# Optimization experiments

Measured on AMD Instinct MI355X. Metric: run time of the kernel, lower is better.

## Reference

```python
import jax, jax.numpy as jnp
import numpy as np

N_NODES = 10000
N_EDGES = 640000
D = 128


def setup_inputs() -> dict:
    key = jax.random.key(0)
    ks = jax.random.split(key, 8)
    x = jax.random.normal(ks[0], (N_NODES, D), dtype=jnp.float32)
    edge_weight = jax.random.uniform(ks[1], (N_EDGES,), dtype=jnp.float32)
    W0 = jax.random.normal(ks[2], (D, D), dtype=jnp.float32) * (1.0 / np.sqrt(D))
    b0 = jnp.zeros((D,), dtype=jnp.float32)
    W1 = jax.random.normal(ks[3], (D, D), dtype=jnp.float32) * (1.0 / np.sqrt(D))
    b1 = jnp.zeros((D,), dtype=jnp.float32)
    src = jax.random.randint(ks[4], (N_EDGES,), 0, N_NODES)
    dst = jax.random.randint(ks[5], (N_EDGES,), 0, N_NODES)
    return {"x": x, "edge_weight": edge_weight, "W0": W0, "b0": b0,
            "W1": W1, "b1": b1, "src": src, "dst": dst}


def _graph_conv(h, src, dst, edge_weight, W, b):
    # DGL GraphConv with norm='both', bias, activation=relu.
    n = h.shape[0]
    ones = jnp.ones((src.shape[0],), dtype=h.dtype)
    out_deg = jax.ops.segment_sum(ones, src, num_segments=n)
    in_deg = jax.ops.segment_sum(ones, dst, num_segments=n)
    norm_src = jax.lax.rsqrt(jnp.maximum(out_deg, 1.0))  # [N]
    norm_dst = jax.lax.rsqrt(jnp.maximum(in_deg, 1.0))   # [N]
    h = h * norm_src[:, None]
    # gather -> weight edges -> scatter-add (sparse neighbor aggregation)
    msg = h[src] * edge_weight[:, None]                  # [E, D]
    agg = jax.ops.segment_sum(msg, dst, num_segments=n)  # [N, D]
    rst = agg @ W                                        # in_feats == out_feats: aggregate first
    rst = rst * norm_dst[:, None] + b
    return jax.nn.relu(rst)  # activation inside GraphConv


def reference(x, edge_weight, W0, b0, W1, b1, src, dst):
    # NET.forward (full-graph path): per layer GraphConv -> activation -> dropout.
    # Dropout is identity in eval mode; outer relu after GraphConv's internal relu is idempotent
    # but applied for faithfulness.
    h = jax.nn.relu(_graph_conv(x, src, dst, edge_weight, W0, b0))
    h = jax.nn.relu(_graph_conv(h, src, dst, edge_weight, W1, b1))
    return h  # predict is None (n_classes=None)
```

## Files before the change

kernel.cpp:

```cpp
#include <hip/hip_runtime.h>
#include <hip/hip_fp16.h>

#define D 128
#define NB 256
#define Q 8
#define BQ (NB / Q)
#define NBINS_MAX 10016
#define GM 32

__global__ __launch_bounds__(256) void cast_kernel(const float* __restrict__ x, __half* __restrict__ xh, int total4) {
    int i = blockIdx.x * 256 + threadIdx.x;
    if (i >= total4) return;
    float4 v = *(const float4*)(x + (size_t)i * 4);
    __half2 a = __floats2half2_rn(v.x, v.y);
    __half2 b = __floats2half2_rn(v.z, v.w);
    *(__half2*)(xh + (size_t)i * 4) = a;
    *(__half2*)(xh + (size_t)i * 4 + 2) = b;
}

__global__ __launch_bounds__(256) void hist_kernel(const int* __restrict__ src, const int* __restrict__ dst,
                                                   int* __restrict__ pd, unsigned short* __restrict__ ps,
                                                   int E, int n) {
    __shared__ int hd[NBINS_MAX];
    __shared__ int hs[NBINS_MAX];
    int b = blockIdx.x, t = threadIdx.x;
    int chunk = (E + NB - 1) / NB;
    int e0 = b * chunk, e1 = min(e0 + chunk, E);
    for (int i = t; i < n; i += 256) { hd[i] = 0; hs[i] = 0; }
    __syncthreads();
    for (int e = e0 + t; e < e1; e += 256) {
        atomicAdd(&hd[dst[e]], 1);
        atomicAdd(&hs[src[e]], 1);
    }
    __syncthreads();
    for (int i = t; i < n; i += 256) {
        pd[(size_t)b * n + i] = hd[i];
        ps[(size_t)b * n + i] = (unsigned short)hs[i];
    }
}

__global__ __launch_bounds__(256) void colscan_kernel(int* __restrict__ pd, const unsigned short* __restrict__ ps,
                                                      int* __restrict__ qtot_d, int* __restrict__ qtot_s, int n) {
    int bin = blockIdx.x * 256 + threadIdx.x;
    int q = blockIdx.y;
    if (bin >= n) return;
    int b0 = q * BQ;
    int run = 0, ssum = 0;
#pragma unroll 8
    for (int j = 0; j < BQ; ++j) {
        size_t idx = (size_t)(b0 + j) * n + bin;
        int v = pd[idx];
        pd[idx] = run;
        run += v;
        ssum += (int)ps[idx];
    }
    qtot_d[(size_t)q * n + bin] = run;
    qtot_s[(size_t)q * n + bin] = ssum;
}

__global__ __launch_bounds__(256) void finalize_kernel(int* __restrict__ qtot_d ,
                                                       const int* __restrict__ qtot_s,
                                                       int* __restrict__ in_deg,
                                                       float* __restrict__ norm_src, float* __restrict__ norm_dst,
                                                       int n) {
    int bin = blockIdx.x * 256 + threadIdx.x;
    if (bin >= n) return;
    int run = 0;
#pragma unroll
    for (int q = 0; q < Q; ++q) {
        size_t i = (size_t)q * n + bin;
        int v = qtot_d[i];
        qtot_d[i] = run;
        run += v;
    }
    in_deg[bin] = run;
    norm_dst[bin] = rsqrtf(fmaxf((float)run, 1.0f));
    int tot = 0;
#pragma unroll
    for (int q = 0; q < Q; ++q) tot += qtot_s[(size_t)q * n + bin];
    norm_src[bin] = rsqrtf(fmaxf((float)tot, 1.0f));
}

__global__ __launch_bounds__(1024) void scan_kernel(const int* __restrict__ in_deg, int* __restrict__ row_start, int n) {
    __shared__ int buf[NBINS_MAX];
    __shared__ int part[1024];
    int t = threadIdx.x;
    for (int i = t; i < n; i += 1024) buf[i] = in_deg[i];
    __syncthreads();
    int ipt = (n + 1023) / 1024;
    int lo = min(t * ipt, n), hi = min(lo + ipt, n);
    int s = 0;
    for (int i = lo; i < hi; ++i) s += buf[i];
    part[t] = s;
    __syncthreads();
    for (int off = 1; off < 1024; off <<= 1) {
        int v = 0;
        if (t >= off) v = part[t - off];
        __syncthreads();
        if (t >= off) part[t] += v;
        __syncthreads();
    }
    int run = part[t] - s;
    for (int i = lo; i < hi; ++i) {
        int v = buf[i];
        buf[i] = run;
        run += v;
    }
    __syncthreads();
    for (int i = t; i < n; i += 1024) row_start[i] = buf[i];
    if (t == 0) row_start[n] = part[1023];
}

__global__ __launch_bounds__(256) void fill_kernel(const int* __restrict__ src, const int* __restrict__ dst,
                                                   const float* __restrict__ ew, const float* __restrict__ ns,
                                                   const int* __restrict__ row_start, const int* __restrict__ qbase,
                                                   const int* __restrict__ pd,
                                                   int2* __restrict__ sorted, int E, int n) {
    __shared__ int cursor[NBINS_MAX];
    int b = blockIdx.x, t = threadIdx.x;
    int q = b / BQ;
    int chunk = (E + NB - 1) / NB;
    int e0 = b * chunk, e1 = min(e0 + chunk, E);
    for (int i = t; i < n; i += 256)
        cursor[i] = row_start[i] + qbase[(size_t)q * n + i] + pd[(size_t)b * n + i];
    __syncthreads();
    for (int e = e0 + t; e < e1; e += 256) {
        int d = dst[e];
        int slot = atomicAdd(&cursor[d], 1);
        int s = src[e];
        int2 rec;
        rec.x = s;
        rec.y = __float_as_int(ew[e] * ns[s]);
        sorted[slot] = rec;
    }
}

__global__ __launch_bounds__(256) void agg_kernel(const __half* __restrict__ h, const int* __restrict__ row_start,
                                                  const int2* __restrict__ sorted, float* __restrict__ out,
                                                  int n, int qn) {
    int slot  = blockIdx.x & 7;
    int g     = blockIdx.x >> 3;
    int chunk = slot >> 2;
    int quad  = slot & 3;
    int wave  = threadIdx.x >> 6;
    int lane  = threadIdx.x & 63;
    int node  = quad * qn + g * 4 + wave;
    int hiN   = min((quad + 1) * qn, n);
    if (node >= hiN) return;
    const __half* hc = h + chunk * 64 + lane;
    int beg = __builtin_amdgcn_readfirstlane(row_start[node]);
    int end = __builtin_amdgcn_readfirstlane(row_start[node + 1]);
    float acc = 0.f;
    int s = beg;
    if (s < end && (s & 1)) {
        int2 rr = sorted[s];
        acc = fmaf(__int_as_float(rr.y), __half2float(hc[(size_t)rr.x << 7]), acc);
        ++s;
    }
    int4 p0, p1, p2, p3, p4, p5, p6, p7;
    if (s + 16 <= end) {
        p0 = *(const int4*)(sorted + s);
        p1 = *(const int4*)(sorted + s + 2);
        p2 = *(const int4*)(sorted + s + 4);
        p3 = *(const int4*)(sorted + s + 6);
        p4 = *(const int4*)(sorted + s + 8);
        p5 = *(const int4*)(sorted + s + 10);
        p6 = *(const int4*)(sorted + s + 12);
        p7 = *(const int4*)(sorted + s + 14);
    }
    for (; s + 32 <= end; s += 16) {
        int4 q0 = *(const int4*)(sorted + s + 16);
        int4 q1 = *(const int4*)(sorted + s + 18);
        int4 q2 = *(const int4*)(sorted + s + 20);
        int4 q3 = *(const int4*)(sorted + s + 22);
        int4 q4 = *(const int4*)(sorted + s + 24);
        int4 q5 = *(const int4*)(sorted + s + 26);
        int4 q6 = *(const int4*)(sorted + s + 28);
        int4 q7 = *(const int4*)(sorted + s + 30);
        __half x0  = hc[(size_t)p0.x << 7];
        __half x1  = hc[(size_t)p0.z << 7];
        __half x2  = hc[(size_t)p1.x << 7];
        __half x3  = hc[(size_t)p1.z << 7];
        __half x4  = hc[(size_t)p2.x << 7];
        __half x5  = hc[(size_t)p2.z << 7];
        __half x6  = hc[(size_t)p3.x << 7];
        __half x7  = hc[(size_t)p3.z << 7];
        __half x8  = hc[(size_t)p4.x << 7];
        __half x9  = hc[(size_t)p4.z << 7];
        __half x10 = hc[(size_t)p5.x << 7];
        __half x11 = hc[(size_t)p5.z << 7];
        __half x12 = hc[(size_t)p6.x << 7];
        __half x13 = hc[(size_t)p6.z << 7];
        __half x14 = hc[(size_t)p7.x << 7];
        __half x15 = hc[(size_t)p7.z << 7];
        acc = fmaf(__int_as_float(p0.y), __half2float(x0),  acc);
        acc = fmaf(__int_as_float(p0.w), __half2float(x1),  acc);
        acc = fmaf(__int_as_float(p1.y), __half2float(x2),  acc);
        acc = fmaf(__int_as_float(p1.w), __half2float(x3),  acc);
        acc = fmaf(__int_as_float(p2.y), __half2float(x4),  acc);
        acc = fmaf(__int_as_float(p2.w), __half2float(x5),  acc);
        acc = fmaf(__int_as_float(p3.y), __half2float(x6),  acc);
        acc = fmaf(__int_as_float(p3.w), __half2float(x7),  acc);
        acc = fmaf(__int_as_float(p4.y), __half2float(x8),  acc);
        acc = fmaf(__int_as_float(p4.w), __half2float(x9),  acc);
        acc = fmaf(__int_as_float(p5.y), __half2float(x10), acc);
        acc = fmaf(__int_as_float(p5.w), __half2float(x11), acc);
        acc = fmaf(__int_as_float(p6.y), __half2float(x12), acc);
        acc = fmaf(__int_as_float(p6.w), __half2float(x13), acc);
        acc = fmaf(__int_as_float(p7.y), __half2float(x14), acc);
        acc = fmaf(__int_as_float(p7.w), __half2float(x15), acc);
        p0 = q0; p1 = q1; p2 = q2; p3 = q3;
        p4 = q4; p5 = q5; p6 = q6; p7 = q7;
    }
    if (s + 16 <= end) {
        acc = fmaf(__int_as_float(p0.y), __half2float(hc[(size_t)p0.x << 7]), acc);
        acc = fmaf(__int_as_float(p0.w), __half2float(hc[(size_t)p0.z << 7]), acc);
        acc = fmaf(__int_as_float(p1.y), __half2float(hc[(size_t)p1.x << 7]), acc);
        acc = fmaf(__int_as_float(p1.w), __half2float(hc[(size_t)p1.z << 7]), acc);
        acc = fmaf(__int_as_float(p2.y), __half2float(hc[(size_t)p2.x << 7]), acc);
        acc = fmaf(__int_as_float(p2.w), __half2float(hc[(size_t)p2.z << 7]), acc);
        acc = fmaf(__int_as_float(p3.y), __half2float(hc[(size_t)p3.x << 7]), acc);
        acc = fmaf(__int_as_float(p3.w), __half2float(hc[(size_t)p3.z << 7]), acc);
        acc = fmaf(__int_as_float(p4.y), __half2float(hc[(size_t)p4.x << 7]), acc);
        acc = fmaf(__int_as_float(p4.w), __half2float(hc[(size_t)p4.z << 7]), acc);
        acc = fmaf(__int_as_float(p5.y), __half2float(hc[(size_t)p5.x << 7]), acc);
        acc = fmaf(__int_as_float(p5.w), __half2float(hc[(size_t)p5.z << 7]), acc);
        acc = fmaf(__int_as_float(p6.y), __half2float(hc[(size_t)p6.x << 7]), acc);
        acc = fmaf(__int_as_float(p6.w), __half2float(hc[(size_t)p6.z << 7]), acc);
        acc = fmaf(__int_as_float(p7.y), __half2float(hc[(size_t)p7.x << 7]), acc);
        acc = fmaf(__int_as_float(p7.w), __half2float(hc[(size_t)p7.z << 7]), acc);
        s += 16;
    }
    if (s + 8 <= end) {
        int4 a0 = *(const int4*)(sorted + s);
        int4 a1 = *(const int4*)(sorted + s + 2);
        int4 a2 = *(const int4*)(sorted + s + 4);
        int4 a3 = *(const int4*)(sorted + s + 6);
        acc = fmaf(__int_as_float(a0.y), __half2float(hc[(size_t)a0.x << 7]), acc);
        acc = fmaf(__int_as_float(a0.w), __half2float(hc[(size_t)a0.z << 7]), acc);
        acc = fmaf(__int_as_float(a1.y), __half2float(hc[(size_t)a1.x << 7]), acc);
        acc = fmaf(__int_as_float(a1.w), __half2float(hc[(size_t)a1.z << 7]), acc);
        acc = fmaf(__int_as_float(a2.y), __half2float(hc[(size_t)a2.x << 7]), acc);
        acc = fmaf(__int_as_float(a2.w), __half2float(hc[(size_t)a2.z << 7]), acc);
        acc = fmaf(__int_as_float(a3.y), __half2float(hc[(size_t)a3.x << 7]), acc);
        acc = fmaf(__int_as_float(a3.w), __half2float(hc[(size_t)a3.z << 7]), acc);
        s += 8;
    }
    for (; s + 2 <= end; s += 2) {
        int4 p = *(const int4*)(sorted + s);
        acc = fmaf(__int_as_float(p.y), __half2float(hc[(size_t)p.x << 7]), acc);
        acc = fmaf(__int_as_float(p.w), __half2float(hc[(size_t)p.z << 7]), acc);
    }
    if (s < end) {
        int2 rr = sorted[s];
        acc = fmaf(__int_as_float(rr.y), __half2float(hc[(size_t)rr.x << 7]), acc);
    }
    out[((size_t)node << 7) + chunk * 64 + lane] = acc;
}

template <int HALF_OUT>
__global__ __launch_bounds__(256) void gemm_kernel(const float* __restrict__ A, const float* __restrict__ W,
                                                   const float* __restrict__ bias, const float* __restrict__ norm_dst,
                                                   float* __restrict__ out, __half* __restrict__ out_h, int n) {
    __shared__ __align__(16) float sAT[D][GM + 2];
    int tid = threadIdx.x;
    int row0 = blockIdx.x * GM;
    for (int i = tid; i < GM * 32; i += 256) {
        int r = i >> 5;
        int kq = i & 31;
        int rr = row0 + r;
        float4 v = make_float4(0.f, 0.f, 0.f, 0.f);
        if (rr < n) v = *(const float4*)(A + (size_t)rr * D + kq * 4);
        sAT[kq * 4 + 0][r] = v.x;
        sAT[kq * 4 + 1][r] = v.y;
        sAT[kq * 4 + 2][r] = v.z;
        sAT[kq * 4 + 3][r] = v.w;
    }
    __syncthreads();
    int tx = tid & 15;
    int ty = tid >> 4;
    int c0 = tx * 8;
    int r0 = ty * 2;
    float acc0[8], acc1[8];
#pragma unroll
    for (int j = 0; j < 8; ++j) { acc0[j] = 0.f; acc1[j] = 0.f; }
    const float* Wk = W + c0;
#pragma unroll 4
    for (int k = 0; k < D; ++k) {
        float2 a = *(const float2*)&sAT[k][r0];
        float4 w0 = *(const float4*)(Wk);
        float4 w1 = *(const float4*)(Wk + 4);
        Wk += D;
        acc0[0] = fmaf(a.x, w0.x, acc0[0]);
        acc0[1] = fmaf(a.x, w0.y, acc0[1]);
        acc0[2] = fmaf(a.x, w0.z, acc0[2]);
        acc0[3] = fmaf(a.x, w0.w, acc0[3]);
        acc0[4] = fmaf(a.x, w1.x, acc0[4]);
        acc0[5] = fmaf(a.x, w1.y, acc0[5]);
        acc0[6] = fmaf(a.x, w1.z, acc0[6]);
        acc0[7] = fmaf(a.x, w1.w, acc0[7]);
        acc1[0] = fmaf(a.y, w0.x, acc1[0]);
        acc1[1] = fmaf(a.y, w0.y, acc1[1]);
        acc1[2] = fmaf(a.y, w0.z, acc1[2]);
        acc1[3] = fmaf(a.y, w0.w, acc1[3]);
        acc1[4] = fmaf(a.y, w1.x, acc1[4]);
        acc1[5] = fmaf(a.y, w1.y, acc1[5]);
        acc1[6] = fmaf(a.y, w1.z, acc1[6]);
        acc1[7] = fmaf(a.y, w1.w, acc1[7]);
    }
#pragma unroll 2
    for (int rr = 0; rr < 2; ++rr) {
        int r = row0 + r0 + rr;
        if (r >= n) continue;
        float* acc = rr ? acc1 : acc0;
        float nd = norm_dst[r];
        float o[8];
#pragma unroll
        for (int j = 0; j < 8; ++j) o[j] = fmaxf(fmaf(acc[j], nd, bias[c0 + j]), 0.f);
        if (HALF_OUT) {
            __half2 h0 = __floats2half2_rn(o[0], o[1]);
            __half2 h1 = __floats2half2_rn(o[2], o[3]);
            __half2 h2 = __floats2half2_rn(o[4], o[5]);
            __half2 h3 = __floats2half2_rn(o[6], o[7]);
            __half* p = out_h + (size_t)r * D + c0;
            *(__half2*)(p + 0) = h0;
            *(__half2*)(p + 2) = h1;
            *(__half2*)(p + 4) = h2;
            *(__half2*)(p + 6) = h3;
        } else {
            float4 o0 = make_float4(o[0], o[1], o[2], o[3]);
            float4 o1 = make_float4(o[4], o[5], o[6], o[7]);
            *(float4*)(out + (size_t)r * D + c0) = o0;
            *(float4*)(out + (size_t)r * D + c0 + 4) = o1;
        }
    }
}

extern "C" void kernel_launch(void* const* d_in, const int* in_sizes, int n_in,
                              void* d_out, int out_size, void* d_ws, size_t ws_size,
                              hipStream_t stream) {
    const float* x  = (const float*)d_in[0];
    const float* ew = (const float*)d_in[1];
    const float* W0 = (const float*)d_in[2];
    const float* b0 = (const float*)d_in[3];
    const float* W1 = (const float*)d_in[4];
    const float* b1 = (const float*)d_in[5];
    const int* src  = (const int*)d_in[6];
    const int* dst  = (const int*)d_in[7];
    float* out = (float*)d_out;

    int n = in_sizes[0] / D;
    int E = in_sizes[6];
    if (n <= 0 || E <= 0) return;

    char* ws = (char*)d_ws;
    size_t off = 0;
    auto alloc = [&](size_t bytes) -> void* {
        void* p = ws + off;
        off = (off + bytes + 255) & ~(size_t)255;
        return p;
    };
    int* row_start  = (int*)alloc(((size_t)n + 1) * 4);
    int* in_deg     = (int*)alloc((size_t)n * 4);
    float* norm_src = (float*)alloc((size_t)n * 4);
    float* norm_dst = (float*)alloc((size_t)n * 4);
    int* qtot_d     = (int*)alloc((size_t)Q * n * 4);
    int* qtot_s     = (int*)alloc((size_t)Q * n * 4);
    int2* sorted    = (int2*)alloc((size_t)E * 8);
    int* pd         = (int*)alloc((size_t)NB * n * 4);
    unsigned short* ps = (unsigned short*)alloc((size_t)NB * n * 2);
    float* B1       = (float*)alloc((size_t)n * D * 4);
    __half* xh      = (__half*)alloc((size_t)n * D * 2);
    __half* B2h     = (__half*)alloc((size_t)n * D * 2);

    int nb = (n + 255) / 256;
    int qn = (n + 3) / 4;
    int ab = 8 * ((qn + 3) / 4);
    int gb = (n + GM - 1) / GM;
    int cb = ((n * D / 4) + 255) / 256;

    cast_kernel<<<cb, 256, 0, stream>>>(x, xh, n * D / 4);
    hist_kernel<<<NB, 256, 0, stream>>>(src, dst, pd, ps, E, n);
    colscan_kernel<<<dim3(nb, Q), 256, 0, stream>>>(pd, ps, qtot_d, qtot_s, n);
    finalize_kernel<<<nb, 256, 0, stream>>>(qtot_d, qtot_s, in_deg, norm_src, norm_dst, n);
    scan_kernel<<<1, 1024, 0, stream>>>(in_deg, row_start, n);
    fill_kernel<<<NB, 256, 0, stream>>>(src, dst, ew, norm_src, row_start, qtot_d, pd, sorted, E, n);

    agg_kernel<<<ab, 256, 0, stream>>>(xh, row_start, sorted, B1, n, qn);
    gemm_kernel<1><<<gb, 256, 0, stream>>>(B1, W0, b0, norm_dst, nullptr, B2h, n);
    agg_kernel<<<ab, 256, 0, stream>>>(B2h, row_start, sorted, B1, n, qn);
    gemm_kernel<0><<<gb, 256, 0, stream>>>(B1, W1, b1, norm_dst, out, nullptr, n);
}
```

Measured before the change: 188.5 us.

## Fuse neighbor aggregation and dense GEMM into one per-layer kernel

Aggregation results for a 32-node tile are now written straight into shared memory and consumed by the GEMM epilogue in the same block, replacing the separate agg and gemm kernels. This removes the fp32 intermediate buffer round-trip through global memory and two kernel launches. Blocks grow to 512 threads, with each wave handling 8 row-chunk tasks serially. The grid shrinks to about 313 blocks, and the old node-quadrant interleaving across blocks is gone, which may reduce latency hiding and load balance for the gather phase.

```diff
diff --git a/kernel.cpp b/kernel.cpp
--- a/kernel.cpp
+++ b/kernel.cpp
@@ -135,21 +135,8 @@
     }
 }
 
-__global__ __launch_bounds__(256) void agg_kernel(const __half* __restrict__ h, const int* __restrict__ row_start,
-                                                  const int2* __restrict__ sorted, float* __restrict__ out,
-                                                  int n, int qn) {
-    int slot  = blockIdx.x & 7;
-    int g     = blockIdx.x >> 3;
-    int chunk = slot >> 2;
-    int quad  = slot & 3;
-    int wave  = threadIdx.x >> 6;
-    int lane  = threadIdx.x & 63;
-    int node  = quad * qn + g * 4 + wave;
-    int hiN   = min((quad + 1) * qn, n);
-    if (node >= hiN) return;
-    const __half* hc = h + chunk * 64 + lane;
-    int beg = __builtin_amdgcn_readfirstlane(row_start[node]);
-    int end = __builtin_amdgcn_readfirstlane(row_start[node + 1]);
+__device__ __forceinline__ float agg_row(const __half* __restrict__ hc, const int2* __restrict__ sorted,
+                                         int beg, int end) {
     float acc = 0.f;
     int s = beg;
     if (s < end && (s & 1)) {
@@ -255,64 +242,59 @@
         int2 rr = sorted[s];
         acc = fmaf(__int_as_float(rr.y), __half2float(hc[(size_t)rr.x << 7]), acc);
     }
-    out[((size_t)node << 7) + chunk * 64 + lane] = acc;
+    return acc;
 }
 
 template <int HALF_OUT>
-__global__ __launch_bounds__(256) void gemm_kernel(const float* __restrict__ A, const float* __restrict__ W,
-                                                   const float* __restrict__ bias, const float* __restrict__ norm_dst,
-                                                   float* __restrict__ out, __half* __restrict__ out_h, int n) {
+__global__ __launch_bounds__(512) void fused_kernel(const __half* __restrict__ h, const int* __restrict__ row_start,
+                                                    const int2* __restrict__ sorted,
+                                                    const float* __restrict__ W, const float* __restrict__ bias,
+                                                    const float* __restrict__ norm_dst,
+                                                    float* __restrict__ out, __half* __restrict__ out_h, int n) {
     __shared__ __align__(16) float sAT[D][GM + 2];
-    int tid = threadIdx.x;
+    int tid  = threadIdx.x;
+    int wave = tid >> 6;
+    int lane = tid & 63;
     int row0 = blockIdx.x * GM;
-    for (int i = tid; i < GM * 32; i += 256) {
-        int r = i >> 5;
-        int kq = i & 31;
-        int rr = row0 + r;
-        float4 v = make_float4(0.f, 0.f, 0.f, 0.f);
-        if (rr < n) v = *(const float4*)(A + (size_t)rr * D + kq * 4);
-        sAT[kq * 4 + 0][r] = v.x;
-        sAT[kq * 4 + 1][r] = v.y;
-        sAT[kq * 4 + 2][r] = v.z;
-        sAT[kq * 4 + 3][r] = v.w;
+#pragma unroll 1
+    for (int t = 0; t < 8; ++t) {
+        int task  = wave * 8 + t;
+        int r     = task & 31;
+        int chunk = task >> 5;
+        int node  = row0 + r;
+        if (node < n) {
+            const __half* hc = h + chunk * 64 + lane;
+            int beg = __builtin_amdgcn_readfirstlane(row_start[node]);
+            int end = __builtin_amdgcn_readfirstlane(row_start[node + 1]);
+            float acc = agg_row(hc, sorted, beg, end);
+            sAT[chunk * 64 + lane][r] = acc;
+        }
     }
     __syncthreads();
     int tx = tid & 15;
     int ty = tid >> 4;
     int c0 = tx * 8;
-    int r0 = ty * 2;
-    float acc0[8], acc1[8];
+    float acc[8];
 #pragma unroll
-    for (int j = 0; j < 8; ++j) { acc0[j] = 0.f; acc1[j] = 0.f; }
+    for (int j = 0; j < 8; ++j) acc[j] = 0.f;
     const float* Wk = W + c0;
 #pragma unroll 4
     for (int k = 0; k < D; ++k) {
-        float2 a = *(const float2*)&sAT[k][r0];
+        float a = sAT[k][ty];
         float4 w0 = *(const float4*)(Wk);
         float4 w1 = *(const float4*)(Wk + 4);
         Wk += D;
-        acc0[0] = fmaf(a.x, w0.x, acc0[0]);
-        acc0[1] = fmaf(a.x, w0.y, acc0[1]);
-        acc0[2] = fmaf(a.x, w0.z, acc0[2]);
-        acc0[3] = fmaf(a.x, w0.w, acc0[3]);
-        acc0[4] = fmaf(a.x, w1.x, acc0[4]);
-        acc0[5] = fmaf(a.x, w1.y, acc0[5]);
-        acc0[6] = fmaf(a.x, w1.z, acc0[6]);
-        acc0[7] = fmaf(a.x, w1.w, acc0[7]);
-        acc1[0] = fmaf(a.y, w0.x, acc1[0]);
-        acc1[1] = fmaf(a.y, w0.y, acc1[1]);
-        acc1[2] = fmaf(a.y, w0.z, acc1[2]);
-        acc1[3] = fmaf(a.y, w0.w, acc1[3]);
-        acc1[4] = fmaf(a.y, w1.x, acc1[4]);
-        acc1[5] = fmaf(a.y, w1.y, acc1[5]);
-        acc1[6] = fmaf(a.y, w1.z, acc1[6]);
-        acc1[7] = fmaf(a.y, w1.w, acc1[7]);
-    }
-#pragma unroll 2
-    for (int rr = 0; rr < 2; ++rr) {
-        int r = row0 + r0 + rr;
-        if (r >= n) continue;
-        float* acc = rr ? acc1 : acc0;
+        acc[0] = fmaf(a, w0.x, acc[0]);
+        acc[1] = fmaf(a, w0.y, acc[1]);
+        acc[2] = fmaf(a, w0.z, acc[2]);
+        acc[3] = fmaf(a, w0.w, acc[3]);
+        acc[4] = fmaf(a, w1.x, acc[4]);
+        acc[5] = fmaf(a, w1.y, acc[5]);
+        acc[6] = fmaf(a, w1.z, acc[6]);
+        acc[7] = fmaf(a, w1.w, acc[7]);
+    }
+    int r = row0 + ty;
+    if (r < n) {
         float nd = norm_dst[r];
         float o[8];
 #pragma unroll
@@ -328,10 +310,8 @@
             *(__half2*)(p + 4) = h2;
             *(__half2*)(p + 6) = h3;
         } else {
-            float4 o0 = make_float4(o[0], o[1], o[2], o[3]);
-            float4 o1 = make_float4(o[4], o[5], o[6], o[7]);
-            *(float4*)(out + (size_t)r * D + c0) = o0;
-            *(float4*)(out + (size_t)r * D + c0 + 4) = o1;
+            *(float4*)(out + (size_t)r * D + c0)     = make_float4(o[0], o[1], o[2], o[3]);
+            *(float4*)(out + (size_t)r * D + c0 + 4) = make_float4(o[4], o[5], o[6], o[7]);
         }
     }
 }
@@ -369,13 +349,10 @@
     int2* sorted    = (int2*)alloc((size_t)E * 8);
     int* pd         = (int*)alloc((size_t)NB * n * 4);
     unsigned short* ps = (unsigned short*)alloc((size_t)NB * n * 2);
-    float* B1       = (float*)alloc((size_t)n * D * 4);
     __half* xh      = (__half*)alloc((size_t)n * D * 2);
     __half* B2h     = (__half*)alloc((size_t)n * D * 2);
 
     int nb = (n + 255) / 256;
-    int qn = (n + 3) / 4;
-    int ab = 8 * ((qn + 3) / 4);
     int gb = (n + GM - 1) / GM;
     int cb = ((n * D / 4) + 255) / 256;
 
@@ -386,8 +363,6 @@
     scan_kernel<<<1, 1024, 0, stream>>>(in_deg, row_start, n);
     fill_kernel<<<NB, 256, 0, stream>>>(src, dst, ew, norm_src, row_start, qtot_d, pd, sorted, E, n);
 
-    agg_kernel<<<ab, 256, 0, stream>>>(xh, row_start, sorted, B1, n, qn);
-    gemm_kernel<1><<<gb, 256, 0, stream>>>(B1, W0, b0, norm_dst, nullptr, B2h, n);
-    agg_kernel<<<ab, 256, 0, stream>>>(B2h, row_start, sorted, B1, n, qn);
-    gemm_kernel<0><<<gb, 256, 0, stream>>>(B1, W1, b1, norm_dst, out, nullptr, n);
-}
+    fused_kernel<1><<<gb, 512, 0, stream>>>(xh, row_start, sorted, W0, b0, norm_dst, nullptr, B2h, n);
+    fused_kernel<0><<<gb, 512, 0, stream>>>(B2h, row_start, sorted, W1, b1, norm_dst, out, nullptr, n);
+}
```

Result: slower. 237.9 us (+26.2%).

## Fuse degree finalize and row scan into one decoupled-lookback kernel, vectorize histogram passes

Applied to the files above, without the earlier changes.

Merges the finalize and single-block scan kernels into one multi-block scan. Blocks chain their prefix through a global counter with spin-waiting, and the kernel also writes per-quarter row bases so fill_kernel no longer adds row_start. The histogram, column-scan and fill cursor setup now use int4 vectorized accesses, so colscan gets four bins per thread. This cuts one launch and the serial 1024-thread scan, but the spin-wait assumes blocks are scheduled in order and needs a memset of the counter.

```diff
diff --git a/kernel.cpp b/kernel.cpp
--- a/kernel.cpp
+++ b/kernel.cpp
@@ -21,19 +21,33 @@
 __global__ __launch_bounds__(256) void hist_kernel(const int* __restrict__ src, const int* __restrict__ dst,
                                                    int* __restrict__ pd, unsigned short* __restrict__ ps,
                                                    int E, int n) {
-    __shared__ int hd[NBINS_MAX];
-    __shared__ int hs[NBINS_MAX];
+    __shared__ __align__(16) int hd[NBINS_MAX];
+    __shared__ __align__(16) int hs[NBINS_MAX];
     int b = blockIdx.x, t = threadIdx.x;
     int chunk = (E + NB - 1) / NB;
     int e0 = b * chunk, e1 = min(e0 + chunk, E);
-    for (int i = t; i < n; i += 256) { hd[i] = 0; hs[i] = 0; }
+    int nq = (n + 3) >> 2;
+    for (int i = t; i < nq; i += 256) {
+        *(int4*)(&hd[i * 4]) = make_int4(0, 0, 0, 0);
+        *(int4*)(&hs[i * 4]) = make_int4(0, 0, 0, 0);
+    }
     __syncthreads();
     for (int e = e0 + t; e < e1; e += 256) {
         atomicAdd(&hd[dst[e]], 1);
         atomicAdd(&hs[src[e]], 1);
     }
     __syncthreads();
-    for (int i = t; i < n; i += 256) {
+    int nf = n >> 2;
+    for (int i = t; i < nf; i += 256) {
+        int4 h = *(const int4*)(&hd[i * 4]);
+        *(int4*)(pd + (size_t)b * n + i * 4) = h;
+        int4 s = *(const int4*)(&hs[i * 4]);
+        uint2 u;
+        u.x = (unsigned)(s.x & 0xFFFF) | ((unsigned)(s.y & 0xFFFF) << 16);
+        u.y = (unsigned)(s.z & 0xFFFF) | ((unsigned)(s.w & 0xFFFF) << 16);
+        *(uint2*)(ps + (size_t)b * n + i * 4) = u;
+    }
+    for (int i = nf * 4 + t; i < n; i += 256) {
         pd[(size_t)b * n + i] = hd[i];
         ps[(size_t)b * n + i] = (unsigned short)hs[i];
     }
@@ -41,88 +55,144 @@
 
 __global__ __launch_bounds__(256) void colscan_kernel(int* __restrict__ pd, const unsigned short* __restrict__ ps,
                                                       int* __restrict__ qtot_d, int* __restrict__ qtot_s, int n) {
-    int bin = blockIdx.x * 256 + threadIdx.x;
+    int bin4 = (blockIdx.x * 256 + threadIdx.x) * 4;
     int q = blockIdx.y;
-    if (bin >= n) return;
+    if (bin4 >= n) return;
     int b0 = q * BQ;
-    int run = 0, ssum = 0;
+    if (bin4 + 3 < n) {
+        int4 run = make_int4(0, 0, 0, 0);
+        int4 ssum = make_int4(0, 0, 0, 0);
 #pragma unroll 8
-    for (int j = 0; j < BQ; ++j) {
-        size_t idx = (size_t)(b0 + j) * n + bin;
-        int v = pd[idx];
-        pd[idx] = run;
-        run += v;
-        ssum += (int)ps[idx];
-    }
-    qtot_d[(size_t)q * n + bin] = run;
-    qtot_s[(size_t)q * n + bin] = ssum;
-}
-
-__global__ __launch_bounds__(256) void finalize_kernel(int* __restrict__ qtot_d ,
-                                                       const int* __restrict__ qtot_s,
-                                                       int* __restrict__ in_deg,
-                                                       float* __restrict__ norm_src, float* __restrict__ norm_dst,
-                                                       int n) {
-    int bin = blockIdx.x * 256 + threadIdx.x;
-    if (bin >= n) return;
-    int run = 0;
-#pragma unroll
-    for (int q = 0; q < Q; ++q) {
-        size_t i = (size_t)q * n + bin;
-        int v = qtot_d[i];
-        qtot_d[i] = run;
-        run += v;
-    }
-    in_deg[bin] = run;
-    norm_dst[bin] = rsqrtf(fmaxf((float)run, 1.0f));
-    int tot = 0;
-#pragma unroll
-    for (int q = 0; q < Q; ++q) tot += qtot_s[(size_t)q * n + bin];
-    norm_src[bin] = rsqrtf(fmaxf((float)tot, 1.0f));
-}
-
-__global__ __launch_bounds__(1024) void scan_kernel(const int* __restrict__ in_deg, int* __restrict__ row_start, int n) {
-    __shared__ int buf[NBINS_MAX];
-    __shared__ int part[1024];
-    int t = threadIdx.x;
-    for (int i = t; i < n; i += 1024) buf[i] = in_deg[i];
-    __syncthreads();
-    int ipt = (n + 1023) / 1024;
-    int lo = min(t * ipt, n), hi = min(lo + ipt, n);
-    int s = 0;
-    for (int i = lo; i < hi; ++i) s += buf[i];
-    part[t] = s;
-    __syncthreads();
-    for (int off = 1; off < 1024; off <<= 1) {
-        int v = 0;
-        if (t >= off) v = part[t - off];
+        for (int j = 0; j < BQ; ++j) {
+            size_t idx = (size_t)(b0 + j) * n + bin4;
+            int4 v = *(const int4*)(pd + idx);
+            *(int4*)(pd + idx) = run;
+            run.x += v.x; run.y += v.y; run.z += v.z; run.w += v.w;
+            uint2 u = *(const uint2*)(ps + idx);
+            ssum.x += (int)(u.x & 0xFFFF); ssum.y += (int)(u.x >> 16);
+            ssum.z += (int)(u.y & 0xFFFF); ssum.w += (int)(u.y >> 16);
+        }
+        *(int4*)(qtot_d + (size_t)q * n + bin4) = run;
+        *(int4*)(qtot_s + (size_t)q * n + bin4) = ssum;
+    } else {
+        for (int bin = bin4; bin < n; ++bin) {
+            int run = 0, ssum = 0;
+            for (int j = 0; j < BQ; ++j) {
+                size_t idx = (size_t)(b0 + j) * n + bin;
+                int v = pd[idx];
+                pd[idx] = run;
+                run += v;
+                ssum += (int)ps[idx];
+            }
+            qtot_d[(size_t)q * n + bin] = run;
+            qtot_s[(size_t)q * n + bin] = ssum;
+        }
+    }
+}
+
+__global__ __launch_bounds__(256) void finscan_kernel(int* __restrict__ qtot_d, const int* __restrict__ qtot_s,
+                                                      int* __restrict__ row_start,
+                                                      float* __restrict__ norm_src, float* __restrict__ norm_dst,
+                                                      int* __restrict__ lb, int n) {
+    __shared__ int part[256];
+    __shared__ int sbase;
+    int t = threadIdx.x, blk = blockIdx.x;
+    int b4 = (blk * 256 + t) * 4;
+    int cnt = (b4 < n) ? min(4, n - b4) : 0;
+    int4 qv[Q];
+    int deg[4] = {0, 0, 0, 0};
+    if (cnt == 4) {
+#pragma unroll
+        for (int q = 0; q < Q; ++q) {
+            qv[q] = *(const int4*)(qtot_d + (size_t)q * n + b4);
+            deg[0] += qv[q].x; deg[1] += qv[q].y; deg[2] += qv[q].z; deg[3] += qv[q].w;
+        }
+    } else if (cnt > 0) {
+#pragma unroll
+        for (int q = 0; q < Q; ++q) {
+            int* c = (int*)&qv[q];
+            for (int j = 0; j < 4; ++j) c[j] = 0;
+            for (int j = 0; j < cnt; ++j) {
+                c[j] = qtot_d[(size_t)q * n + b4 + j];
+                deg[j] += c[j];
+            }
+        }
+    }
+    int tot = deg[0] + deg[1] + deg[2] + deg[3];
+    part[t] = tot;
+    __syncthreads();
+    for (int off = 1; off < 256; off <<= 1) {
+        int v = (t >= off) ? part[t - off] : 0;
         __syncthreads();
         if (t >= off) part[t] += v;
         __syncthreads();
     }
-    int run = part[t] - s;
-    for (int i = lo; i < hi; ++i) {
-        int v = buf[i];
-        buf[i] = run;
-        run += v;
-    }
-    __syncthreads();
-    for (int i = t; i < n; i += 1024) row_start[i] = buf[i];
-    if (t == 0) row_start[n] = part[1023];
+    int thread_excl = part[t] - tot;
+    int block_tot = part[255];
+    if (t == 0) {
+        while (atomicAdd(&lb[0], 0) != blk) { }
+        __threadfence();
+        int running = atomicAdd(&lb[1], block_tot);
+        __threadfence();
+        atomicExch(&lb[0], blk + 1);
+        sbase = running;
+    }
+    __syncthreads();
+    if (cnt == 0) return;
+    int base = sbase + thread_excl;
+    int rs[4];
+    int run = base;
+    for (int j = 0; j < cnt; ++j) { rs[j] = run; run += deg[j]; }
+    if (cnt == 4) *(int4*)(row_start + b4) = make_int4(rs[0], rs[1], rs[2], rs[3]);
+    else for (int j = 0; j < cnt; ++j) row_start[b4 + j] = rs[j];
+    if (b4 + cnt == n) row_start[n] = run;
+    for (int j = 0; j < cnt; ++j) norm_dst[b4 + j] = rsqrtf(fmaxf((float)deg[j], 1.0f));
+    int stot[4] = {0, 0, 0, 0};
+    if (cnt == 4) {
+#pragma unroll
+        for (int q = 0; q < Q; ++q) {
+            int4 v = *(const int4*)(qtot_s + (size_t)q * n + b4);
+            stot[0] += v.x; stot[1] += v.y; stot[2] += v.z; stot[3] += v.w;
+        }
+    } else {
+#pragma unroll
+        for (int q = 0; q < Q; ++q)
+            for (int j = 0; j < cnt; ++j) stot[j] += qtot_s[(size_t)q * n + b4 + j];
+    }
+    for (int j = 0; j < cnt; ++j) norm_src[b4 + j] = rsqrtf(fmaxf((float)stot[j], 1.0f));
+    int qrun[4] = {rs[0], rs[1], rs[2], rs[3]};
+#pragma unroll
+    for (int q = 0; q < Q; ++q) {
+        if (cnt == 4) {
+            *(int4*)(qtot_d + (size_t)q * n + b4) = make_int4(qrun[0], qrun[1], qrun[2], qrun[3]);
+            qrun[0] += qv[q].x; qrun[1] += qv[q].y; qrun[2] += qv[q].z; qrun[3] += qv[q].w;
+        } else {
+            int* c = (int*)&qv[q];
+            for (int j = 0; j < cnt; ++j) {
+                qtot_d[(size_t)q * n + b4 + j] = qrun[j];
+                qrun[j] += c[j];
+            }
+        }
+    }
 }
 
 __global__ __launch_bounds__(256) void fill_kernel(const int* __restrict__ src, const int* __restrict__ dst,
                                                    const float* __restrict__ ew, const float* __restrict__ ns,
-                                                   const int* __restrict__ row_start, const int* __restrict__ qbase,
-                                                   const int* __restrict__ pd,
+                                                   const int* __restrict__ qrow, const int* __restrict__ pd,
                                                    int2* __restrict__ sorted, int E, int n) {
-    __shared__ int cursor[NBINS_MAX];
+    __shared__ __align__(16) int cursor[NBINS_MAX];
     int b = blockIdx.x, t = threadIdx.x;
     int q = b / BQ;
     int chunk = (E + NB - 1) / NB;
     int e0 = b * chunk, e1 = min(e0 + chunk, E);
-    for (int i = t; i < n; i += 256)
-        cursor[i] = row_start[i] + qbase[(size_t)q * n + i] + pd[(size_t)b * n + i];
+    int nf = n >> 2;
+    for (int i = t; i < nf; i += 256) {
+        int4 a = *(const int4*)(qrow + (size_t)q * n + i * 4);
+        int4 c = *(const int4*)(pd + (size_t)b * n + i * 4);
+        *(int4*)(&cursor[i * 4]) = make_int4(a.x + c.x, a.y + c.y, a.z + c.z, a.w + c.w);
+    }
+    for (int i = nf * 4 + t; i < n; i += 256)
+        cursor[i] = qrow[(size_t)q * n + i] + pd[(size_t)b * n + i];
     __syncthreads();
     for (int e = e0 + t; e < e1; e += 256) {
         int d = dst[e];
@@ -361,7 +431,7 @@
         return p;
     };
     int* row_start  = (int*)alloc(((size_t)n + 1) * 4);
-    int* in_deg     = (int*)alloc((size_t)n * 4);
+    int* lb         = (int*)alloc(2 * 4);
     float* norm_src = (float*)alloc((size_t)n * 4);
     float* norm_dst = (float*)alloc((size_t)n * 4);
     int* qtot_d     = (int*)alloc((size_t)Q * n * 4);
@@ -373,18 +443,18 @@
     __half* xh      = (__half*)alloc((size_t)n * D * 2);
     __half* B2h     = (__half*)alloc((size_t)n * D * 2);
 
-    int nb = (n + 255) / 256;
+    int nb4 = (n + 1023) / 1024;
     int qn = (n + 3) / 4;
     int ab = 8 * ((qn + 3) / 4);
     int gb = (n + GM - 1) / GM;
     int cb = ((n * D / 4) + 255) / 256;
 
+    hipMemsetAsync(lb, 0, 8, stream);
     cast_kernel<<<cb, 256, 0, stream>>>(x, xh, n * D / 4);
     hist_kernel<<<NB, 256, 0, stream>>>(src, dst, pd, ps, E, n);
-    colscan_kernel<<<dim3(nb, Q), 256, 0, stream>>>(pd, ps, qtot_d, qtot_s, n);
-    finalize_kernel<<<nb, 256, 0, stream>>>(qtot_d, qtot_s, in_deg, norm_src, norm_dst, n);
-    scan_kernel<<<1, 1024, 0, stream>>>(in_deg, row_start, n);
-    fill_kernel<<<NB, 256, 0, stream>>>(src, dst, ew, norm_src, row_start, qtot_d, pd, sorted, E, n);
+    colscan_kernel<<<dim3(nb4, Q), 256, 0, stream>>>(pd, ps, qtot_d, qtot_s, n);
+    finscan_kernel<<<nb4, 256, 0, stream>>>(qtot_d, qtot_s, row_start, norm_src, norm_dst, lb, n);
+    fill_kernel<<<NB, 256, 0, stream>>>(src, dst, ew, norm_src, qtot_d, pd, sorted, E, n);
 
     agg_kernel<<<ab, 256, 0, stream>>>(xh, row_start, sorted, B1, n, qn);
     gemm_kernel<1><<<gb, 256, 0, stream>>>(B1, W0, b0, norm_dst, nullptr, B2h, n);
```

Measured after the change: 200.6 us. 6.4% more time.
